# Kernel optimization log

Measured on AMD Instinct MI355X. Metric: run time of the kernel, lower is better.

Reference implementation:

```python
import jax, jax.numpy as jnp
import numpy as np

C = 64      # in_planes == mid_planes == out_planes (see notes: required for shape consistency)
K = 16      # nsample == k (KNN neighbors)
N = 32768   # number of points
B = 1       # batch (forward only type-checks for B==1 or B==k)


def _bn(x, g, b):
    # inference-mode BatchNorm1d: running_mean=0, running_var=1, eps=1e-5; channel = last axis
    return x * (g / jnp.sqrt(1.0 + 1e-5)) + b


def setup_inputs():
    ks = jax.random.split(jax.random.key(0), 33)
    f = lambda i, s: jax.random.normal(ks[i], s, jnp.float32) * 0.05
    # neighbor indices: global indices into the flattened (B*N) point set; avoid self-loops
    # so degenerate zero-length edges (0/0 divisions) only occur with prob ~0
    rel = jax.random.randint(ks[3], (N, K), 1, N)
    idx = ((jnp.arange(N)[:, None] + rel) % N).reshape(B, N, K)
    return dict(
        x=jax.random.normal(ks[0], (B, C, N), jnp.float32),
        y=jax.random.normal(ks[1], (B, C, N), jnp.float32),
        y_xyz=jax.random.uniform(ks[2], (B, 3, N), dtype=jnp.float32),
        idx=idx,
        Wq=f(4, (C, C)), bq=f(5, (C,)),
        Wk=f(6, (C, C)), bk=f(7, (C,)),
        Wv=f(8, (C, C)), bv=f(9, (C,)),
        Wu=f(10, (C, 1)), bu=f(11, (1,)), gu=jnp.ones((1,), jnp.float32), bnu=f(12, (1,)),
        Wp1=f(13, (3, 3)), bp1=f(14, (3,)), gp=jnp.ones((3,), jnp.float32), bnp=f(15, (3,)),
        Wp2=f(16, (3, C)), bp2=f(17, (C,)),
        Wa1=f(18, (3, 3)), ba1=f(19, (3,)), ga=jnp.ones((3,), jnp.float32), bna=f(20, (3,)),
        Wa2=f(21, (3, C)), ba2=f(22, (C,)),
        gw1=jnp.ones((C,), jnp.float32), bw1b=f(23, (C,)), Ww1=f(24, (C, C)), bw1=f(25, (C,)),
        gw2=jnp.ones((C,), jnp.float32), bw2b=f(26, (C,)), Ww2=f(27, (C, C)), bw2=f(28, (C,)),
        a_p=f(29, (K, 1)), b_p=f(30, (K, C)), d_p=f(31, (K, C)),
    )


def reference(x, y, y_xyz, idx, Wq, bq, Wk, bk, Wv, bv, Wu, bu, gu, bnu,
              Wp1, bp1, gp, bnp, Wp2, bp2, Wa1, ba1, ga, bna, Wa2, ba2,
              gw1, bw1b, Ww1, bw1, gw2, bw2b, Ww2, bw2, a_p, b_p, d_p):
    b_, cin, n = x.shape
    p = jnp.transpose(y_xyz, (0, 2, 1)).reshape(b_ * n, 3)      # (N,3) coordinates
    y_r = jnp.transpose(y, (0, 2, 1))                            # (B,n,C)
    xt = jnp.transpose(x, (0, 2, 1)).reshape(b_ * n, cin)
    yt = y_r.reshape(b_ * n, cin)
    x_q = xt @ Wq + bq                                           # (N,C)
    y_k_all = yt @ Wk + bk                                       # (N,C)
    y_v_all = yt @ Wv + bv                                       # (N,C)
    # note: original uses x.reshape(-1, C) (NOT a transpose) -- kept faithfully
    x_uni = jax.nn.relu(_bn(x.reshape(-1, cin) @ Wu + bu, gu, bnu))  # (N,1)
    idxf = idx.reshape(b_ * n, -1)                               # (N,K) global neighbor idx
    pos = p[idxf] - p[:, None, :]                                # (N,K,3) relative coords
    y_kg = y_k_all[idxf]                                         # (N,K,C) gathered keys
    y_vg = y_v_all[idxf]                                         # (N,K,C) gathered values
    # distances computed on detached positions in the original (numpy round-trip)
    pos_sg = jax.lax.stop_gradient(pos)
    e_dis = jnp.linalg.norm(pos_sg, axis=2, keepdims=True)       # (N,K,1)
    e_dis_xy = jnp.linalg.norm(pos_sg[:, :, :2], axis=2, keepdims=True)
    cos_e = jnp.nan_to_num(e_dis_xy / e_dis)
    cos_a = jnp.nan_to_num(pos[:, :, 1:2] / e_dis_xy)
    all_feat = jnp.concatenate([e_dis, cos_a, cos_e], axis=-1)   # (N,K,3)
    all_feat = jax.nn.relu(_bn(all_feat @ Wa1 + ba1, ga, bna)) @ Wa2 + ba2  # (N,K,C)
    p_r = jax.nn.relu(_bn(pos @ Wp1 + bp1, gp, bnp)) @ Wp2 + bp2           # (N,K,C)
    p_r = p_r + d_p * all_feat
    # dual softmax attention
    diff = y_kg - x_q[:, None, :]                                # (N,K,C)
    w_d = jax.nn.softmax(jnp.einsum('nkc,n->ck', diff, x_uni[:, 0]), axis=1)  # (C,K)
    w_e = jax.nn.softmax(jnp.einsum('nc,ck->nk', y_r[0], w_d)[:, :, None], axis=1)  # (N,K,1)
    w = a_p * w_d.T[None] + b_p * w_e                            # (N,K,C)
    w = jax.nn.relu(_bn(w, gw1, bw1b)) @ Ww1 + bw1
    w = jax.nn.relu(_bn(w, gw2, bw2b)) @ Ww2 + bw2
    w = jax.nn.softmax(w, axis=1)                                # softmax over neighbors
    return ((y_vg + p_r) * w).sum(axis=1)                        # (N,C)
```

## Files before the change

kernel.cpp:

```cpp
#include <hip/hip_runtime.h>
#include <hip/hip_bf16.h>
#include <math.h>

#define NPTS 32768
#define C 64
#define K 16
#define NB2 512
#define NB2R 64
#define NTAB 512
#define BN_INV 0.99999500003749968f

__device__ __forceinline__ float safediv_n2n(float a, float b) {
    float q = a / b;
    if (isnan(q)) return 0.0f;
    if (isinf(q)) return copysignf(3.402823466e38f, q);
    return q;
}

__device__ __forceinline__ float bf16_to_f(ushort u) {
    return __uint_as_float((unsigned)u << 16);
}

__global__ __launch_bounds__(256) void proj3_kernel(
    const float* __restrict__ x, const float* __restrict__ y,
    const float* __restrict__ Wq, const float* __restrict__ bq,
    const float* __restrict__ Wk, const float* __restrict__ bk,
    const float* __restrict__ Wv, const float* __restrict__ bv,
    float* __restrict__ xq, __hip_bfloat16* __restrict__ ykb,
    __hip_bfloat16* __restrict__ yvb)
{
    const int dir = blockIdx.y;
    const float* __restrict__ in   = (dir == 0) ? x  : y;
    const float* __restrict__ W    = (dir == 0) ? Wq : (dir == 1) ? Wk : Wv;
    const float* __restrict__ bias = (dir == 0) ? bq : (dir == 1) ? bk : bv;

    const int lane = threadIdx.x & 63;
    const int wave = threadIdx.x >> 6;
    const int n0 = blockIdx.x * 64;

    __shared__ float hs[C][C];

    #pragma unroll
    for (int i = 0; i < 16; ++i) {
        const int c = i * 4 + wave;
        hs[c][lane] = in[(size_t)c * NPTS + n0 + lane];
    }
    __syncthreads();

    const int p0 = wave * 16;
    float acc[16];
    const float b = bias[lane];
    #pragma unroll
    for (int i = 0; i < 16; ++i) acc[i] = b;

    #pragma unroll
    for (int c = 0; c < C; ++c) {
        const float wcl = W[c * C + lane];
        float va[16];
        ((float4*)va)[0] = *(const float4*)&hs[c][p0];
        ((float4*)va)[1] = *(const float4*)&hs[c][p0 + 4];
        ((float4*)va)[2] = *(const float4*)&hs[c][p0 + 8];
        ((float4*)va)[3] = *(const float4*)&hs[c][p0 + 12];
        #pragma unroll
        for (int i = 0; i < 16; ++i) acc[i] = fmaf(va[i], wcl, acc[i]);
    }

    if (dir == 0) {
        #pragma unroll
        for (int i = 0; i < 16; ++i)
            xq[(size_t)(n0 + p0 + i) * C + lane] = acc[i];
    } else {
        __hip_bfloat16* __restrict__ dst = (dir == 1) ? ykb : yvb;
        #pragma unroll
        for (int i = 0; i < 16; ++i)
            dst[(size_t)(n0 + p0 + i) * C + lane] = __float2bfloat16(acc[i]);
    }
}

__global__ __launch_bounds__(256) void aux_kernel(
    const float* __restrict__ x, const float* __restrict__ y_xyz,
    const float* __restrict__ Wu, const float* __restrict__ bu,
    const float* __restrict__ gu, const float* __restrict__ bnu,
    float* __restrict__ xu, float4* __restrict__ pk)
{
    const int lane = threadIdx.x & 63;
    const int wave = threadIdx.x >> 6;

    const float wul = Wu[lane];
    const float bnscale = gu[0] * BN_INV;
    const float bu0 = bu[0], bnu0 = bnu[0];
    #pragma unroll 4
    for (int i = 0; i < 16; ++i) {
        const int m = blockIdx.x * 64 + wave * 16 + i;
        float v = x[m * 64 + lane] * wul;
        #pragma unroll
        for (int off = 32; off > 0; off >>= 1) v += __shfl_xor(v, off, 64);
        if (lane == 0) {
            float u = (v + bu0) * bnscale + bnu0;
            xu[m] = fmaxf(u, 0.0f);
        }
    }
    if (wave == 0) {
        const int p = blockIdx.x * 64 + lane;
        pk[p] = make_float4(y_xyz[p], y_xyz[NPTS + p], y_xyz[2 * NPTS + p], 0.0f);
    }
}

__global__ __launch_bounds__(256) void sred_kernel(
    const float* __restrict__ xq, const __hip_bfloat16* __restrict__ ykb,
    const float* __restrict__ xu, const int* __restrict__ idx,
    float* __restrict__ partG)
{
    const int lane = threadIdx.x & 63;
    const int wv = __builtin_amdgcn_readfirstlane(threadIdx.x >> 6);
    const int gw = blockIdx.x * 4 + wv;
    const int nwv = NB2 * 4;
    const ushort* __restrict__ yku = (const ushort*)ykb;

    float g[K];
    #pragma unroll
    for (int k = 0; k < K; ++k) g[k] = 0.0f;

    for (int n = gw; n < NPTS; n += nwv) {
        const float xuv = xu[n];
        if (xuv != 0.0f) {
            const float xqv = xq[(size_t)n * C + lane];
            const int4* ir = (const int4*)(idx + (size_t)n * K);
            const int4 i0 = ir[0], i1 = ir[1], i2 = ir[2], i3 = ir[3];
            int ids[K] = { i0.x, i0.y, i0.z, i0.w, i1.x, i1.y, i1.z, i1.w,
                           i2.x, i2.y, i2.z, i2.w, i3.x, i3.y, i3.z, i3.w };
            #pragma unroll
            for (int k = 0; k < K; ++k) {
                const float ykv = bf16_to_f(yku[(size_t)ids[k] * C + lane]);
                g[k] = fmaf(ykv - xqv, xuv, g[k]);
            }
        }
    }

    __shared__ float red[4][K][C];
    #pragma unroll
    for (int k = 0; k < K; ++k) red[wv][k][lane] = g[k];
    __syncthreads();
    if (wv == 0) {
        #pragma unroll
        for (int k = 0; k < K; ++k) {
            float s = red[0][k][lane] + red[1][k][lane] + red[2][k][lane] + red[3][k][lane];
            partG[blockIdx.x * (K * C) + k * C + lane] = s;
        }
    }
}

__global__ __launch_bounds__(1024) void sred2_kernel(
    const float* __restrict__ partG, float* __restrict__ part2)
{
    const int j = blockIdx.x;
    const int t = threadIdx.x;
    float s = 0.0f;
    #pragma unroll
    for (int i = 0; i < NB2 / NB2R; ++i)
        s += partG[(size_t)(j + NB2R * i) * (K * C) + t];
    part2[(size_t)j * (K * C) + t] = s;
}

__global__ __launch_bounds__(1024) void wd_kernel(
    const float* __restrict__ part2, const float* __restrict__ a_p,
    float* __restrict__ wd, float* __restrict__ awdT)
{
    __shared__ float S[K][C];
    const int t = threadIdx.x;
    {
        float s = 0.0f;
        #pragma unroll 8
        for (int b = 0; b < NB2R; ++b) s += part2[b * (K * C) + t];
        S[0][t] = s;
    }
    __syncthreads();
    if (t < C) {
        const int c = t;
        float v[K];
        float m = -3.402823466e38f;
        #pragma unroll
        for (int k = 0; k < K; ++k) { v[k] = S[k][c]; m = fmaxf(m, v[k]); }
        float sum = 0.0f;
        #pragma unroll
        for (int k = 0; k < K; ++k) { v[k] = expf(v[k] - m); sum += v[k]; }
        const float r = 1.0f / sum;
        #pragma unroll
        for (int k = 0; k < K; ++k) {
            const float wv = v[k] * r;
            wd[c * K + k] = wv;
            awdT[k * C + c] = a_p[k] * wv;
        }
    }
}

__global__ __launch_bounds__(256) void we_kernel(
    const float* __restrict__ y, const float* __restrict__ wd,
    float* __restrict__ we)
{
    __shared__ float wds[C][K];
    const int lane = threadIdx.x & 63;
    const int wave = threadIdx.x >> 6;
    for (int i = threadIdx.x; i < C * K; i += 256) wds[0][i] = wd[i];
    __syncthreads();

    const int n = (blockIdx.x * 4 + wave) * 64 + lane;
    float L[K];
    #pragma unroll
    for (int k = 0; k < K; ++k) L[k] = 0.0f;
    for (int c = 0; c < C; ++c) {
        const float yv = y[c * NPTS + n];
        float wa[K];
        ((float4*)wa)[0] = ((const float4*)&wds[c][0])[0];
        ((float4*)wa)[1] = ((const float4*)&wds[c][0])[1];
        ((float4*)wa)[2] = ((const float4*)&wds[c][0])[2];
        ((float4*)wa)[3] = ((const float4*)&wds[c][0])[3];
        #pragma unroll
        for (int k = 0; k < K; ++k) L[k] = fmaf(yv, wa[k], L[k]);
    }
    float m = L[0];
    #pragma unroll
    for (int k = 1; k < K; ++k) m = fmaxf(m, L[k]);
    float sum = 0.0f;
    #pragma unroll
    for (int k = 0; k < K; ++k) { L[k] = expf(L[k] - m); sum += L[k]; }
    const float r = 1.0f / sum;
    float* dst = we + (size_t)n * K;
    ((float4*)dst)[0] = make_float4(L[0]*r, L[1]*r, L[2]*r, L[3]*r);
    ((float4*)dst)[1] = make_float4(L[4]*r, L[5]*r, L[6]*r, L[7]*r);
    ((float4*)dst)[2] = make_float4(L[8]*r, L[9]*r, L[10]*r, L[11]*r);
    ((float4*)dst)[3] = make_float4(L[12]*r, L[13]*r, L[14]*r, L[15]*r);
}

__global__ __launch_bounds__(64) void tab_kernel(
    const float* __restrict__ awdT, const float* __restrict__ b_p,
    const float* __restrict__ Ww1, const float* __restrict__ bw1,
    const float* __restrict__ Ww2, const float* __restrict__ bw2,
    const float* __restrict__ gw1, const float* __restrict__ bw1b,
    const float* __restrict__ gw2, const float* __restrict__ bw2b,
    float* __restrict__ tab)
{
    const int lane = threadIdx.x;
    const int k  = blockIdx.y;
    const int i0 = blockIdx.x * 16;

    const float aw = awdT[k * C + lane];
    const float bp = b_p[k * C + lane];
    const float gs1 = gw1[lane] * BN_INV, bb1 = bw1b[lane], bw1c = bw1[lane];
    const float gs2 = gw2[lane] * BN_INV, bb2 = bw2b[lane], bw2c = bw2[lane];

    float w1c[C], w2c[C];
    #pragma unroll
    for (int c = 0; c < C; ++c) { w1c[c] = Ww1[c * C + lane]; w2c[c] = Ww2[c * C + lane]; }

    __shared__ float hs[16][C];

    #pragma unroll
    for (int r = 0; r < 16; ++r) {
        const float t = (float)(i0 + r) * (1.0f / NTAB);
        const float wv = fmaf(bp, t, aw);
        hs[r][lane] = fmaxf(fmaf(wv, gs1, bb1), 0.0f);
    }
    __syncthreads();

    float o[16];
    #pragma unroll
    for (int r = 0; r < 16; ++r) o[r] = bw1c;
    #pragma unroll
    for (int c4 = 0; c4 < 16; ++c4) {
        #pragma unroll
        for (int r = 0; r < 16; ++r) {
            const float4 hv = *(const float4*)&hs[r][c4 * 4];
            o[r] = fmaf(hv.x, w1c[c4 * 4 + 0], o[r]);
            o[r] = fmaf(hv.y, w1c[c4 * 4 + 1], o[r]);
            o[r] = fmaf(hv.z, w1c[c4 * 4 + 2], o[r]);
            o[r] = fmaf(hv.w, w1c[c4 * 4 + 3], o[r]);
        }
    }
    __syncthreads();
    #pragma unroll
    for (int r = 0; r < 16; ++r)
        hs[r][lane] = fmaxf(fmaf(o[r], gs2, bb2), 0.0f);
    __syncthreads();
    #pragma unroll
    for (int r = 0; r < 16; ++r) o[r] = bw2c;
    #pragma unroll
    for (int c4 = 0; c4 < 16; ++c4) {
        #pragma unroll
        for (int r = 0; r < 16; ++r) {
            const float4 hv = *(const float4*)&hs[r][c4 * 4];
            o[r] = fmaf(hv.x, w2c[c4 * 4 + 0], o[r]);
            o[r] = fmaf(hv.y, w2c[c4 * 4 + 1], o[r]);
            o[r] = fmaf(hv.z, w2c[c4 * 4 + 2], o[r]);
            o[r] = fmaf(hv.w, w2c[c4 * 4 + 3], o[r]);
        }
    }
    #pragma unroll
    for (int r = 0; r < 16; ++r) {
        const int i = i0 + r;
        if (i <= NTAB) tab[(k * (NTAB + 1) + i) * C + lane] = o[r];
    }
}

__global__ __launch_bounds__(256, 5) void main4_kernel(
    const int* __restrict__ idx, const float4* __restrict__ pk,
    const __hip_bfloat16* __restrict__ yvb, const float* __restrict__ we,
    const float* __restrict__ tab, const float* __restrict__ d_p,
    const float* __restrict__ Wa1, const float* __restrict__ ba1,
    const float* __restrict__ ga, const float* __restrict__ bna,
    const float* __restrict__ Wa2, const float* __restrict__ ba2,
    const float* __restrict__ Wp1, const float* __restrict__ bp1,
    const float* __restrict__ gp, const float* __restrict__ bnp,
    const float* __restrict__ Wp2, const float* __restrict__ bp2,
    float* __restrict__ out)
{
    const int lane = threadIdx.x & 63;
    const int wv = __builtin_amdgcn_readfirstlane(threadIdx.x >> 6);
    const int n = blockIdx.x * 4 + wv;

    __shared__ float geo[4][K][8];
    __shared__ float prm[36];

    if (threadIdx.x < 36) {
        const int t = threadIdx.x;
        float v;
        if (t < 9)       v = Wa1[t];
        else if (t < 12) v = ba1[t - 9];
        else if (t < 21) v = Wp1[t - 12];
        else if (t < 24) v = bp1[t - 21];
        else if (t < 27) v = ga[t - 24];
        else if (t < 30) v = bna[t - 27];
        else if (t < 33) v = gp[t - 30];
        else             v = bnp[t - 33];
        prm[t] = v;
    }
    __syncthreads();

    const int4* ir = (const int4*)(idx + (size_t)n * K);
    const int4 i0 = ir[0], i1 = ir[1], i2 = ir[2], i3 = ir[3];
    const int ids[K] = { i0.x, i0.y, i0.z, i0.w, i1.x, i1.y, i1.z, i1.w,
                         i2.x, i2.y, i2.z, i2.w, i3.x, i3.y, i3.z, i3.w };
    const float4 self = pk[n];
    const float4 wv0 = ((const float4*)(we + (size_t)n * K))[0];
    const float4 wv1 = ((const float4*)(we + (size_t)n * K))[1];
    const float4 wv2 = ((const float4*)(we + (size_t)n * K))[2];
    const float4 wv3 = ((const float4*)(we + (size_t)n * K))[3];
    const float wearr[K] = { wv0.x, wv0.y, wv0.z, wv0.w, wv1.x, wv1.y, wv1.z, wv1.w,
                             wv2.x, wv2.y, wv2.z, wv2.w, wv3.x, wv3.y, wv3.z, wv3.w };

    const ushort* __restrict__ yvu_base = (const ushort*)yvb;
    ushort yvu[K];
    #pragma unroll
    for (int k = 0; k < K; ++k)
        yvu[k] = yvu_base[(size_t)ids[k] * C + lane];

    {
        const int idv = (idx + (size_t)n * K)[lane & 15];
        const float4 nb = pk[idv];
        const float px = nb.x - self.x;
        const float py = nb.y - self.y;
        const float pz = nb.z - self.z;
        const float ed  = sqrtf(px * px + py * py + pz * pz);
        const float exy = sqrtf(px * px + py * py);
        const float cose = safediv_n2n(exy, ed);
        const float cosa = safediv_n2n(py, exy);
        float gv[6];
        #pragma unroll
        for (int d = 0; d < 3; ++d) {
            const float a = ed * prm[d] + cosa * prm[3 + d] + cose * prm[6 + d] + prm[9 + d];
            gv[d] = fmaxf(a * (prm[24 + d] * BN_INV) + prm[27 + d], 0.0f);
            const float p = px * prm[12 + d] + py * prm[15 + d] + pz * prm[18 + d] + prm[21 + d];
            gv[3 + d] = fmaxf(p * (prm[30 + d] * BN_INV) + prm[33 + d], 0.0f);
        }
        if (lane < K) {
            float* g = &geo[wv][lane][0];
            g[1] = gv[0]; g[2] = gv[1]; g[3] = gv[2];
            g[4] = gv[3]; g[5] = gv[4]; g[6] = gv[5];
        }
    }

    float w2[K];
    #pragma unroll
    for (int h = 0; h < 2; ++h) {
        float tv0[8], tv1[8], fr[8];
        #pragma unroll
        for (int j = 0; j < 8; ++j) {
            const int k = h * 8 + j;
            const float u = wearr[k] * (float)NTAB;
            int ic = (int)u;
            ic = (ic < 0) ? 0 : (ic > NTAB - 1 ? NTAB - 1 : ic);
            fr[j] = u - (float)ic;
            const float* tp = tab + ((size_t)(k * (NTAB + 1) + ic) << 6) + lane;
            tv0[j] = tp[0];
            tv1[j] = tp[C];
        }
        #pragma unroll
        for (int j = 0; j < 8; ++j)
            w2[h * 8 + j] = fmaf(fr[j], tv1[j] - tv0[j], tv0[j]);
    }

    float m = w2[0];
    #pragma unroll
    for (int k = 1; k < K; ++k) m = fmaxf(m, w2[k]);
    float sum = 0.0f;
    #pragma unroll
    for (int k = 0; k < K; ++k) { w2[k] = __expf(w2[k] - m); sum += w2[k]; }
    const float r = 1.0f / sum;

    const float ba2c = ba2[lane], bp2c = bp2[lane];
    float wa2c[3], wp2c[3];
    #pragma unroll
    for (int d = 0; d < 3; ++d) { wa2c[d] = Wa2[d * C + lane]; wp2c[d] = Wp2[d * C + lane]; }

    float acc = 0.0f;
    #pragma unroll
    for (int k = 0; k < K; ++k) {
        const float4 g0 = *(const float4*)&geo[wv][k][0];
        const float4 g1 = *(const float4*)&geo[wv][k][4];
        const float afc = fmaf(g0.y, wa2c[0], fmaf(g0.z, wa2c[1], fmaf(g0.w, wa2c[2], ba2c)));
        float prc = fmaf(g1.x, wp2c[0], fmaf(g1.y, wp2c[1], fmaf(g1.z, wp2c[2], bp2c)));
        prc = fmaf(d_p[k * C + lane], afc, prc);
        acc = fmaf(bf16_to_f(yvu[k]) + prc, w2[k] * r, acc);
    }
    out[(size_t)n * C + lane] = acc;
}

extern "C" void kernel_launch(void* const* d_in, const int* in_sizes, int n_in,
                              void* d_out, int out_size, void* d_ws, size_t ws_size,
                              hipStream_t stream)
{
    (void)in_sizes; (void)n_in; (void)out_size; (void)ws_size;
    const float* x     = (const float*)d_in[0];
    const float* y     = (const float*)d_in[1];
    const float* y_xyz = (const float*)d_in[2];
    const int*   idx   = (const int*)d_in[3];
    const float* Wq = (const float*)d_in[4];  const float* bq = (const float*)d_in[5];
    const float* Wk = (const float*)d_in[6];  const float* bk = (const float*)d_in[7];
    const float* Wv = (const float*)d_in[8];  const float* bv = (const float*)d_in[9];
    const float* Wu = (const float*)d_in[10]; const float* bu = (const float*)d_in[11];
    const float* gu = (const float*)d_in[12]; const float* bnu = (const float*)d_in[13];
    const float* Wp1 = (const float*)d_in[14]; const float* bp1 = (const float*)d_in[15];
    const float* gp  = (const float*)d_in[16]; const float* bnp = (const float*)d_in[17];
    const float* Wp2 = (const float*)d_in[18]; const float* bp2 = (const float*)d_in[19];
    const float* Wa1 = (const float*)d_in[20]; const float* ba1 = (const float*)d_in[21];
    const float* ga  = (const float*)d_in[22]; const float* bna = (const float*)d_in[23];
    const float* Wa2 = (const float*)d_in[24]; const float* ba2 = (const float*)d_in[25];
    const float* gw1 = (const float*)d_in[26]; const float* bw1b = (const float*)d_in[27];
    const float* Ww1 = (const float*)d_in[28]; const float* bw1 = (const float*)d_in[29];
    const float* gw2 = (const float*)d_in[30]; const float* bw2b = (const float*)d_in[31];
    const float* Ww2 = (const float*)d_in[32]; const float* bw2 = (const float*)d_in[33];
    const float* a_p = (const float*)d_in[34];
    const float* b_p = (const float*)d_in[35];
    const float* d_p = (const float*)d_in[36];
    float* out = (float*)d_out;

    float* ws = (float*)d_ws;
    float* xq    = ws;
    float* we    = ws;
    float* tab   = ws + 2097152;
    __hip_bfloat16* ykb = (__hip_bfloat16*)(ws + 2622464);
    __hip_bfloat16* yvb = (__hip_bfloat16*)(ws + 3671040);
    float4* pk   = (float4*)(ws + 4719616);
    float* xu    = ws + 4850688;
    float* partG = ws + 4883456;
    float* part2 = ws + 5407744;
    float* wd    = ws + 5473280;
    float* awdT  = ws + 5474304;

    proj3_kernel<<<dim3(NPTS / 64, 3), 256, 0, stream>>>(
        x, y, Wq, bq, Wk, bk, Wv, bv, xq, ykb, yvb);
    aux_kernel<<<NPTS / 64, 256, 0, stream>>>(x, y_xyz, Wu, bu, gu, bnu, xu, pk);
    sred_kernel<<<NB2, 256, 0, stream>>>(xq, ykb, xu, idx, partG);
    sred2_kernel<<<NB2R, 1024, 0, stream>>>(partG, part2);
    wd_kernel<<<1, 1024, 0, stream>>>(part2, a_p, wd, awdT);
    we_kernel<<<NPTS / 256, 256, 0, stream>>>(y, wd, we);
    tab_kernel<<<dim3(33, 16), 64, 0, stream>>>(awdT, b_p, Ww1, bw1, Ww2, bw2,
                                                gw1, bw1b, gw2, bw2b, tab);
    main4_kernel<<<NPTS / 4, 256, 0, stream>>>(idx, pk, yvb, we, tab, d_p,
        Wa1, ba1, ga, bna, Wa2, ba2, Wp1, bp1, gp, bnp, Wp2, bp2, out);
}
```

Measured before the change: 112.5 us.

## Eliminate query projection via linearity of the xu-weighted diff reduction

The per-point query projection xq is no longer materialized. Instead, sum_n xu[n]*xq[n] is computed as Wq^T(sum_n xu[n]*x[n]) + bq*sum xu, using a small reduction kernel and a fix-up in wd_kernel. This removes an N×C fp32 write and the per-point xq read in sred. The K and V projections are fused into one pass sharing the y tile, with the aux work merged into the same launch. Reassociating the sum into a subtraction of large totals may change floating-point rounding.

Result: slower. 132.3 us (+17.6%).

```diff
diff --git a/kernel.cpp b/kernel.cpp
--- a/kernel.cpp
+++ b/kernel.cpp
@@ -21,93 +21,106 @@
     return __uint_as_float((unsigned)u << 16);
 }
 
-__global__ __launch_bounds__(256) void proj3_kernel(
+__global__ __launch_bounds__(256) void prep_kernel(
     const float* __restrict__ x, const float* __restrict__ y,
-    const float* __restrict__ Wq, const float* __restrict__ bq,
+    const float* __restrict__ y_xyz,
     const float* __restrict__ Wk, const float* __restrict__ bk,
     const float* __restrict__ Wv, const float* __restrict__ bv,
-    float* __restrict__ xq, __hip_bfloat16* __restrict__ ykb,
-    __hip_bfloat16* __restrict__ yvb)
-{
-    const int dir = blockIdx.y;
-    const float* __restrict__ in   = (dir == 0) ? x  : y;
-    const float* __restrict__ W    = (dir == 0) ? Wq : (dir == 1) ? Wk : Wv;
-    const float* __restrict__ bias = (dir == 0) ? bq : (dir == 1) ? bk : bv;
-
+    const float* __restrict__ Wu, const float* __restrict__ bu,
+    const float* __restrict__ gu, const float* __restrict__ bnu,
+    __hip_bfloat16* __restrict__ ykb, __hip_bfloat16* __restrict__ yvb,
+    float* __restrict__ xu, float4* __restrict__ pk)
+{
     const int lane = threadIdx.x & 63;
     const int wave = threadIdx.x >> 6;
+
+    if (blockIdx.y == 1) {
+        const float wul = Wu[lane];
+        const float bnscale = gu[0] * BN_INV;
+        const float bu0 = bu[0], bnu0 = bnu[0];
+        #pragma unroll 4
+        for (int i = 0; i < 16; ++i) {
+            const int m = blockIdx.x * 64 + wave * 16 + i;
+            float v = x[m * 64 + lane] * wul;
+            #pragma unroll
+            for (int off = 32; off > 0; off >>= 1) v += __shfl_xor(v, off, 64);
+            if (lane == 0) {
+                float u = (v + bu0) * bnscale + bnu0;
+                xu[m] = fmaxf(u, 0.0f);
+            }
+        }
+        if (wave == 0) {
+            const int p = blockIdx.x * 64 + lane;
+            pk[p] = make_float4(y_xyz[p], y_xyz[NPTS + p], y_xyz[2 * NPTS + p], 0.0f);
+        }
+        return;
+    }
+
     const int n0 = blockIdx.x * 64;
-
     __shared__ float hs[C][C];
 
     #pragma unroll
     for (int i = 0; i < 16; ++i) {
         const int c = i * 4 + wave;
-        hs[c][lane] = in[(size_t)c * NPTS + n0 + lane];
+        hs[c][lane] = y[(size_t)c * NPTS + n0 + lane];
     }
     __syncthreads();
 
     const int p0 = wave * 16;
-    float acc[16];
-    const float b = bias[lane];
-    #pragma unroll
-    for (int i = 0; i < 16; ++i) acc[i] = b;
+    float acck[16], accv[16];
+    const float bkl = bk[lane], bvl = bv[lane];
+    #pragma unroll
+    for (int i = 0; i < 16; ++i) { acck[i] = bkl; accv[i] = bvl; }
 
     #pragma unroll
     for (int c = 0; c < C; ++c) {
-        const float wcl = W[c * C + lane];
+        const float wkl = Wk[c * C + lane];
+        const float wvl = Wv[c * C + lane];
         float va[16];
         ((float4*)va)[0] = *(const float4*)&hs[c][p0];
         ((float4*)va)[1] = *(const float4*)&hs[c][p0 + 4];
         ((float4*)va)[2] = *(const float4*)&hs[c][p0 + 8];
         ((float4*)va)[3] = *(const float4*)&hs[c][p0 + 12];
         #pragma unroll
-        for (int i = 0; i < 16; ++i) acc[i] = fmaf(va[i], wcl, acc[i]);
-    }
-
-    if (dir == 0) {
-        #pragma unroll
-        for (int i = 0; i < 16; ++i)
-            xq[(size_t)(n0 + p0 + i) * C + lane] = acc[i];
+        for (int i = 0; i < 16; ++i) {
+            acck[i] = fmaf(va[i], wkl, acck[i]);
+            accv[i] = fmaf(va[i], wvl, accv[i]);
+        }
+    }
+
+    #pragma unroll
+    for (int i = 0; i < 16; ++i) {
+        ykb[(size_t)(n0 + p0 + i) * C + lane] = __float2bfloat16(acck[i]);
+        yvb[(size_t)(n0 + p0 + i) * C + lane] = __float2bfloat16(accv[i]);
+    }
+}
+
+__global__ __launch_bounds__(256) void xvec_kernel(
+    const float* __restrict__ x, const float* __restrict__ xu,
+    float* __restrict__ xvec)
+{
+    const int j = blockIdx.x;
+    const int t = threadIdx.x;
+    float s = 0.0f;
+    if (j < C) {
+        const float* __restrict__ row = x + (size_t)j * NPTS;
+        for (int n = t; n < NPTS; n += 256) s = fmaf(row[n], xu[n], s);
     } else {
-        __hip_bfloat16* __restrict__ dst = (dir == 1) ? ykb : yvb;
-        #pragma unroll
-        for (int i = 0; i < 16; ++i)
-            dst[(size_t)(n0 + p0 + i) * C + lane] = __float2bfloat16(acc[i]);
-    }
-}
-
-__global__ __launch_bounds__(256) void aux_kernel(
-    const float* __restrict__ x, const float* __restrict__ y_xyz,
-    const float* __restrict__ Wu, const float* __restrict__ bu,
-    const float* __restrict__ gu, const float* __restrict__ bnu,
-    float* __restrict__ xu, float4* __restrict__ pk)
-{
-    const int lane = threadIdx.x & 63;
-    const int wave = threadIdx.x >> 6;
-
-    const float wul = Wu[lane];
-    const float bnscale = gu[0] * BN_INV;
-    const float bu0 = bu[0], bnu0 = bnu[0];
-    #pragma unroll 4
-    for (int i = 0; i < 16; ++i) {
-        const int m = blockIdx.x * 64 + wave * 16 + i;
-        float v = x[m * 64 + lane] * wul;
-        #pragma unroll
-        for (int off = 32; off > 0; off >>= 1) v += __shfl_xor(v, off, 64);
-        if (lane == 0) {
-            float u = (v + bu0) * bnscale + bnu0;
-            xu[m] = fmaxf(u, 0.0f);
-        }
-    }
-    if (wave == 0) {
-        const int p = blockIdx.x * 64 + lane;
-        pk[p] = make_float4(y_xyz[p], y_xyz[NPTS + p], y_xyz[2 * NPTS + p], 0.0f);
-    }
+        for (int n = t; n < NPTS; n += 256) s += xu[n];
+    }
+    __shared__ float red[256];
+    red[t] = s;
+    __syncthreads();
+    #pragma unroll
+    for (int off = 128; off > 0; off >>= 1) {
+        if (t < off) red[t] += red[t + off];
+        __syncthreads();
+    }
+    if (t == 0) xvec[j] = red[0];
 }
 
 __global__ __launch_bounds__(256) void sred_kernel(
-    const float* __restrict__ xq, const __hip_bfloat16* __restrict__ ykb,
+    const __hip_bfloat16* __restrict__ ykb,
     const float* __restrict__ xu, const int* __restrict__ idx,
     float* __restrict__ partG)
 {
@@ -124,7 +137,6 @@
     for (int n = gw; n < NPTS; n += nwv) {
         const float xuv = xu[n];
         if (xuv != 0.0f) {
-            const float xqv = xq[(size_t)n * C + lane];
             const int4* ir = (const int4*)(idx + (size_t)n * K);
             const int4 i0 = ir[0], i1 = ir[1], i2 = ir[2], i3 = ir[3];
             int ids[K] = { i0.x, i0.y, i0.z, i0.w, i1.x, i1.y, i1.z, i1.w,
@@ -132,7 +144,7 @@
             #pragma unroll
             for (int k = 0; k < K; ++k) {
                 const float ykv = bf16_to_f(yku[(size_t)ids[k] * C + lane]);
-                g[k] = fmaf(ykv - xqv, xuv, g[k]);
+                g[k] = fmaf(ykv, xuv, g[k]);
             }
         }
     }
@@ -163,24 +175,29 @@
 }
 
 __global__ __launch_bounds__(1024) void wd_kernel(
-    const float* __restrict__ part2, const float* __restrict__ a_p,
+    const float* __restrict__ part2, const float* __restrict__ xvec,
+    const float* __restrict__ Wq, const float* __restrict__ bq,
+    const float* __restrict__ a_p,
     float* __restrict__ wd, float* __restrict__ awdT)
 {
     __shared__ float S[K][C];
     const int t = threadIdx.x;
+    const int c = t & 63;
     {
         float s = 0.0f;
         #pragma unroll 8
         for (int b = 0; b < NB2R; ++b) s += part2[b * (K * C) + t];
-        S[0][t] = s;
+        float t1 = bq[c] * xvec[C];
+        #pragma unroll 8
+        for (int j = 0; j < C; ++j) t1 = fmaf(Wq[j * C + c], xvec[j], t1);
+        S[0][t] = s - t1;
     }
     __syncthreads();
     if (t < C) {
-        const int c = t;
         float v[K];
         float m = -3.402823466e38f;
         #pragma unroll
-        for (int k = 0; k < K; ++k) { v[k] = S[k][c]; m = fmaxf(m, v[k]); }
+        for (int k = 0; k < K; ++k) { v[k] = S[k][t]; m = fmaxf(m, v[k]); }
         float sum = 0.0f;
         #pragma unroll
         for (int k = 0; k < K; ++k) { v[k] = expf(v[k] - m); sum += v[k]; }
@@ -188,8 +205,8 @@
         #pragma unroll
         for (int k = 0; k < K; ++k) {
             const float wv = v[k] * r;
-            wd[c * K + k] = wv;
-            awdT[k * C + c] = a_p[k] * wv;
+            wd[t * K + k] = wv;
+            awdT[k * C + t] = a_p[k] * wv;
         }
     }
 }
@@ -455,7 +472,6 @@
     float* out = (float*)d_out;
 
     float* ws = (float*)d_ws;
-    float* xq    = ws;
     float* we    = ws;
     float* tab   = ws + 2097152;
     __hip_bfloat16* ykb = (__hip_bfloat16*)(ws + 2622464);
@@ -466,13 +482,14 @@
     float* part2 = ws + 5407744;
     float* wd    = ws + 5473280;
     float* awdT  = ws + 5474304;
-
-    proj3_kernel<<<dim3(NPTS / 64, 3), 256, 0, stream>>>(
-        x, y, Wq, bq, Wk, bk, Wv, bv, xq, ykb, yvb);
-    aux_kernel<<<NPTS / 64, 256, 0, stream>>>(x, y_xyz, Wu, bu, gu, bnu, xu, pk);
-    sred_kernel<<<NB2, 256, 0, stream>>>(xq, ykb, xu, idx, partG);
+    float* xvec  = ws + 5475328;
+
+    prep_kernel<<<dim3(NPTS / 64, 2), 256, 0, stream>>>(
+        x, y, y_xyz, Wk, bk, Wv, bv, Wu, bu, gu, bnu, ykb, yvb, xu, pk);
+    xvec_kernel<<<C + 1, 256, 0, stream>>>(x, xu, xvec);
+    sred_kernel<<<NB2, 256, 0, stream>>>(ykb, xu, idx, partG);
     sred2_kernel<<<NB2R, 1024, 0, stream>>>(partG, part2);
-    wd_kernel<<<1, 1024, 0, stream>>>(part2, a_p, wd, awdT);
+    wd_kernel<<<1, 1024, 0, stream>>>(part2, xvec, Wq, bq, a_p, wd, awdT);
     we_kernel<<<NPTS / 256, 256, 0, stream>>>(y, wd, we);
     tab_kernel<<<dim3(33, 16), 64, 0, stream>>>(awdT, b_p, Ww1, bw1, Ww2, bw2,
                                                 gw1, bw1b, gw2, bw2b, tab);
```
